# Performance work log

Measured on AMD Instinct MI355X. Metric: run time of the kernel, lower is better.

Reference implementation:

```python
import jax, jax.numpy as jnp
import numpy as np

N, C, H, W = 2, 128, 64, 64
N_HEAD = 4
GROUPS = 16
EPS = 1e-5


def group_norm(x, scale, offset):
    # haiku GroupNorm, channels_first: normalize over (channels-in-group, h, w)
    n, c, h, w = x.shape
    xg = x.reshape(n, GROUPS, c // GROUPS, h, w)
    mu = xg.mean(axis=(2, 3, 4), keepdims=True)
    var = xg.var(axis=(2, 3, 4), keepdims=True)
    xg = (xg - mu) * jax.lax.rsqrt(var + EPS)
    return xg.reshape(n, c, h, w) * scale[None, :, None, None] + offset[None, :, None, None]


def setup_inputs() -> dict:
    key = jax.random.key(0)
    ks = jax.random.split(key, 4)
    inv_sqrt_c = 1.0 / np.sqrt(C).astype(np.float32)
    return {
        "x": jax.random.normal(ks[0], (N, C, H, W), dtype=jnp.float32),
        "w_qkv": jax.random.normal(ks[1], (C, 3 * C), dtype=jnp.float32) * inv_sqrt_c,
        "b_qkv": jnp.zeros((3 * C,), dtype=jnp.float32),
        "w_out": jax.random.normal(ks[2], (C, C), dtype=jnp.float32) * inv_sqrt_c,
        "b_out": jnp.zeros((C,), dtype=jnp.float32),
        "gn1_scale": jnp.ones((C,), dtype=jnp.float32),
        "gn1_offset": jnp.zeros((C,), dtype=jnp.float32),
        "gn2_scale": jnp.ones((C,), dtype=jnp.float32),
        "gn2_offset": jnp.zeros((C,), dtype=jnp.float32),
    }


def reference(x, w_qkv, b_qkv, w_out, b_out, gn1_scale, gn1_offset, gn2_scale, gn2_offset):
    n, c, h, w = x.shape
    dh = c // N_HEAD
    # GroupNorm (x is reassigned, so the residual uses the normalized x)
    xn = group_norm(x, gn1_scale, gn1_offset)
    # 1x1 conv qkv projection: [n, 3c, h, w]
    qkv = jnp.einsum('nchw,cd->ndhw', xn, w_qkv) + b_qkv[None, :, None, None]
    # [n, 3H, dh, hw] -> [n, 3H, hw, dh]
    qkv = jnp.swapaxes(qkv.reshape(n, N_HEAD * 3, dh, h * w), 2, 3)
    q, k, v = jnp.split(qkv, 3, axis=1)  # each [n, H, hw, dh]
    scale = dh ** (-0.25)
    # [n, H, hw, hw] attention matrix (the memory-bound core)
    att = jax.nn.softmax((q * scale) @ (jnp.swapaxes(k, 2, 3) * scale), axis=3)
    y = jnp.swapaxes(att @ v, 2, 3).reshape(n, c, h, w)
    # 1x1 conv out projection + GroupNorm + residual
    out = jnp.einsum('nchw,cd->ndhw', y, w_out) + b_out[None, :, None, None]
    return xn + group_norm(out, gn2_scale, gn2_offset)
```

## Files before the change

### kernel.cpp

```cpp
#include <hip/hip_runtime.h>
#include <hip/hip_bf16.h>
#include <math.h>

constexpr int cHW   = 4096;
constexpr int cC    = 128;
constexpr int cNH   = 4;
constexpr int cDH   = 32;
constexpr float cEPS = 1e-5f;
constexpr float cQS = 0.2550347805f;
constexpr int SPLIT = 4;

typedef short bh8 __attribute__((ext_vector_type(8)));
typedef float f4  __attribute__((ext_vector_type(4)));

static __device__ __forceinline__ unsigned short f2bf(float f) {
  union { __hip_bfloat16 h; unsigned short u; } cv;
  cv.h = __float2bfloat16(f);
  return cv.u;
}
static __device__ __forceinline__ unsigned pack2bf(float a, float b) {
  return (unsigned)f2bf(a) | ((unsigned)f2bf(b) << 16);
}
static __device__ __forceinline__ unsigned pack_trunc(float a, float b) {
  unsigned ua = __builtin_bit_cast(unsigned, a);
  unsigned ub = __builtin_bit_cast(unsigned, b);
  return (ua >> 16) | (ub & 0xffff0000u);
}
static __device__ __forceinline__ float bflo(unsigned pk) {
  return __builtin_bit_cast(float, pk << 16);
}
static __device__ __forceinline__ float bfhi(unsigned pk) {
  return __builtin_bit_cast(float, pk & 0xffff0000u);
}

__device__ __forceinline__ void block_reduce2(float& a, float& b, float* sbuf) {
  #pragma unroll
  for (int off = 32; off > 0; off >>= 1) {
    a += __shfl_down(a, off, 64);
    b += __shfl_down(b, off, 64);
  }
  int wave = threadIdx.x >> 6;
  int lane = threadIdx.x & 63;
  if (lane == 0) { sbuf[wave] = a; sbuf[4 + wave] = b; }
  __syncthreads();
  if (threadIdx.x == 0) {
    sbuf[8] = sbuf[0] + sbuf[1] + sbuf[2] + sbuf[3];
    sbuf[9] = sbuf[4] + sbuf[5] + sbuf[6] + sbuf[7];
  }
  __syncthreads();
  a = sbuf[8];
  b = sbuf[9];
}

__global__ __launch_bounds__(256)
void prep(const float* __restrict__ x, float* __restrict__ part,
          const float* __restrict__ wq, const float* __restrict__ wo,
          unsigned short* __restrict__ wqT, unsigned short* __restrict__ woT) {
  __shared__ float lds[32 * 133];
  int L = threadIdx.x;
  if (blockIdx.x < 256) {
    int ng = blockIdx.x >> 3, sl = blockIdx.x & 7;
    const float4* s4 = (const float4*)x;
    float s = 0.f, s2 = 0.f;
    #pragma unroll
    for (int i = 0; i < 4; i++) {
      int idx = i * 256 + L;
      int c = idx >> 7, tt = idx & 127;
      float4 v = s4[(size_t)(ng * 8 + c) * 1024 + sl * 128 + tt];
      s  += v.x + v.y + v.z + v.w;
      s2 += v.x*v.x + v.y*v.y + v.z*v.z + v.w*v.w;
    }
    block_reduce2(s, s2, lds);
    if (L == 0) { part[blockIdx.x * 2] = s; part[blockIdx.x * 2 + 1] = s2; }
  } else {
    int bx = blockIdx.x - 256;
    const float* src; unsigned short* dst; int W, d0;
    if (bx < 12) { src = wq; dst = wqT; W = 384; d0 = bx * 32; }
    else         { src = wo; dst = woT; W = 128; d0 = (bx - 12) * 32; }
    #pragma unroll
    for (int i = 0; i < 16; i++) {
      int c = i * 8 + (L >> 5), d = L & 31;
      lds[d * 133 + c] = src[(size_t)c * W + d0 + d];
    }
    __syncthreads();
    int d = L >> 3, ch = L & 7, c0 = ch * 16;
    unsigned pk[8];
    #pragma unroll
    for (int j = 0; j < 8; j++)
      pk[j] = pack2bf(lds[d * 133 + c0 + 2 * j], lds[d * 133 + c0 + 2 * j + 1]);
    uint4* d4 = (uint4*)(dst + (size_t)(d0 + d) * 128 + c0);
    d4[0] = make_uint4(pk[0], pk[1], pk[2], pk[3]);
    d4[1] = make_uint4(pk[4], pk[5], pk[6], pk[7]);
  }
}

__global__ __launch_bounds__(256)
void gn_stats(const float* __restrict__ src, float* __restrict__ part) {
  __shared__ float sbuf[10];
  int ng = blockIdx.x >> 3, sl = blockIdx.x & 7;
  const float4* s4 = (const float4*)src;
  float s = 0.f, s2 = 0.f;
  #pragma unroll
  for (int i = 0; i < 4; i++) {
    int idx = i * 256 + threadIdx.x;
    int c = idx >> 7, tt = idx & 127;
    float4 v = s4[(size_t)(ng * 8 + c) * 1024 + sl * 128 + tt];
    s  += v.x + v.y + v.z + v.w;
    s2 += v.x*v.x + v.y*v.y + v.z*v.z + v.w*v.w;
  }
  block_reduce2(s, s2, sbuf);
  if (threadIdx.x == 0) { part[blockIdx.x * 2] = s; part[blockIdx.x * 2 + 1] = s2; }
}

__global__ __launch_bounds__(256)
void gn1_pack(const float* __restrict__ x, const float* __restrict__ part,
              const float* __restrict__ sc, const float* __restrict__ of,
              unsigned short* __restrict__ xnB) {
  int cc = blockIdx.x, ts = blockIdx.y, n = blockIdx.z;
  int ng = n * 16 + cc;
  float s = 0.f, s2 = 0.f;
  #pragma unroll
  for (int p = 0; p < 8; p++) { s += part[(ng*8+p)*2]; s2 += part[(ng*8+p)*2+1]; }
  float mu = s * (1.0f / 32768.0f);
  float rinv = rsqrtf(s2 * (1.0f / 32768.0f) - mu * mu + cEPS);
  int t = ts * 256 + threadIdx.x;
  float v[8];
  #pragma unroll
  for (int j = 0; j < 8; j++) {
    int c = cc * 8 + j;
    float a = rinv * sc[c];
    float bo = of[c] - mu * a;
    v[j] = x[((size_t)n * cC + c) * cHW + t] * a + bo;
  }
  unsigned pk[4];
  #pragma unroll
  for (int j = 0; j < 4; j++) pk[j] = pack2bf(v[2*j], v[2*j+1]);
  ((uint4*)xnB)[(size_t)(n * 16 + cc) * cHW + t] = make_uint4(pk[0], pk[1], pk[2], pk[3]);
}

__global__ __launch_bounds__(256)
void qkv_mfma(const unsigned short* __restrict__ xnB, const unsigned short* __restrict__ wqT,
              const float* __restrict__ bq, unsigned* __restrict__ qB,
              unsigned* __restrict__ kB, unsigned* __restrict__ vI) {
  __shared__ float vbuf[64 * 36];
  const int L = threadIdx.x & 63, w = threadIdx.x >> 6;
  const int c16 = L & 15, q = L >> 4;
  const int t0 = blockIdx.x * 64, dg = blockIdx.y, n = blockIdx.z;
  const int nh = n * 4 + (dg & 3), d0 = dg * 32;
  const f4 zf = {0.f, 0.f, 0.f, 0.f};
  f4 acc0 = zf, acc1 = zf;
  const int trow = t0 + w * 16 + c16;
  #pragma unroll
  for (int ks = 0; ks < 4; ks++) {
    bh8 a  = *(const bh8*)(xnB + ((size_t)(n * 16 + ks * 4 + q) * cHW + trow) * 8);
    bh8 b0 = *(const bh8*)(wqT + (size_t)(d0 + c16) * 128 + ks * 32 + q * 8);
    bh8 b1 = *(const bh8*)(wqT + (size_t)(d0 + 16 + c16) * 128 + ks * 32 + q * 8);
    acc0 = __builtin_amdgcn_mfma_f32_16x16x32_bf16(a, b0, acc0, 0, 0, 0);
    acc1 = __builtin_amdgcn_mfma_f32_16x16x32_bf16(a, b1, acc1, 0, 0, 0);
  }
  float blo = bq[d0 + c16], bhi = bq[d0 + 16 + c16];
  if (dg < 8) {
    float scl = (dg < 4) ? cQS : 1.0f;
    unsigned* dst = (dg < 4) ? qB : kB;
    #pragma unroll
    for (int r = 0; r < 4; r++) {
      unsigned pk = pack2bf((acc0[r] + blo) * scl, (acc1[r] + bhi) * scl);
      dst[((size_t)nh * cHW + t0 + w * 16 + q * 4 + r) * 16 + c16] = pk;
    }
  } else {
    #pragma unroll
    for (int r = 0; r < 4; r++) {
      vbuf[(w * 16 + q * 4 + r) * 36 + c16]      = acc0[r] + blo;
      vbuf[(w * 16 + q * 4 + r) * 36 + 16 + c16] = acc1[r] + bhi;
    }
    __syncthreads();
    int t16 = threadIdx.x & 15, dh8 = (threadIdx.x >> 4) & 15;
    #pragma unroll
    for (int blk = 0; blk < 2; blk++)
      #pragma unroll
      for (int hh = 0; hh < 2; hh++) {
        int dh = dh8 + hh * 16;
        float lo = vbuf[(blk * 32 + t16) * 36 + dh];
        float hi = vbuf[(blk * 32 + 16 + t16) * 36 + dh];
        vI[((size_t)nh * 32 + dh) * 2048 + (size_t)(t0 / 32 + blk) * 16 + t16] = pack2bf(lo, hi);
      }
  }
}

__global__ __launch_bounds__(256)
void flash_mfma(const unsigned short* __restrict__ qB,
                const unsigned short* __restrict__ kB,
                const unsigned short* __restrict__ vI,
                unsigned* __restrict__ opart, float* __restrict__ lpart) {
  __shared__ float pbuf[4][1280];
  const int w = threadIdx.x >> 6, L = threadIdx.x & 63;
  const int c16 = L & 15, q = L >> 4;
  const int qt = blockIdx.x * 4 + w, nh = blockIdx.y, ph = blockIdx.z;
  float* pb = pbuf[w];
  const f4 zf = {0.f, 0.f, 0.f, 0.f};
  const short oneb = 0x3F80;
  const bh8 ones = {oneb, oneb, oneb, oneb, oneb, oneb, oneb, oneb};

  const unsigned short* qb = qB + ((size_t)nh * cHW + qt * 32) * cDH;
  bh8 qa[2];
  qa[0] = *(const bh8*)(qb + (size_t)c16 * cDH + q * 8);
  qa[1] = *(const bh8*)(qb + (size_t)(16 + c16) * cDH + q * 8);

  f4 o[2][2] = {{zf, zf}, {zf, zf}};
  f4 lacc[2] = {zf, zf};

  const unsigned short* kb = kB + (size_t)nh * cHW * cDH;
  const unsigned short* vb = vI + (size_t)nh * cDH * cHW;

  const int kbeg = ph * (cHW / SPLIT);
  const int kend = kbeg + cHW / SPLIT;

  for (int kt = kbeg; kt < kend; kt += 64) {
    bh8 kf[4];
    #pragma unroll
    for (int s = 0; s < 4; s++)
      kf[s] = *(const bh8*)(kb + (size_t)(kt + s*16 + c16) * cDH + q * 8);
    bh8 vf[2][2];
    #pragma unroll
    for (int ks = 0; ks < 2; ks++)
      #pragma unroll
      for (int dt = 0; dt < 2; dt++)
        vf[ks][dt] = *(const bh8*)(vb + (size_t)(dt*16 + c16) * cHW + kt + ks*32 + q*8);

    f4 sf[2][4];
    #pragma unroll
    for (int rt = 0; rt < 2; rt++)
      #pragma unroll
      for (int s = 0; s < 4; s++)
        sf[rt][s] = __builtin_amdgcn_mfma_f32_16x16x32_bf16(qa[rt], kf[s], zf, 0, 0, 0);

    #pragma unroll
    for (int rt = 0; rt < 2; rt++) {
      #pragma unroll
      for (int s = 0; s < 4; s++)
        #pragma unroll
        for (int r = 0; r < 4; r++)
          sf[rt][s][r] = __builtin_amdgcn_exp2f(sf[rt][s][r]);
      #pragma unroll
      for (int st = 0; st < 2; st++)
        #pragma unroll
        for (int r = 0; r < 4; r++) {
          unsigned pk = pack_trunc(sf[rt][2*st][r], sf[rt][2*st+1][r]);
          pb[(rt*2 + st)*320 + (q*4 + r)*20 + c16] = __builtin_bit_cast(float, pk);
        }
    }
    #pragma unroll
    for (int rt = 0; rt < 2; rt++)
      #pragma unroll
      for (int st = 0; st < 2; st++) {
        bh8 pa = *(const bh8*)(pb + (rt*2 + st)*320 + c16*20 + q*4);
        o[rt][0] = __builtin_amdgcn_mfma_f32_16x16x32_bf16(pa, vf[st][0], o[rt][0], 0, 0, 0);
        o[rt][1] = __builtin_amdgcn_mfma_f32_16x16x32_bf16(pa, vf[st][1], o[rt][1], 0, 0, 0);
        lacc[rt] = __builtin_amdgcn_mfma_f32_16x16x32_bf16(pa, ones, lacc[rt], 0, 0, 0);
      }
  }

  size_t base_r = (size_t)ph * 32768 + (size_t)nh * cHW + (size_t)qt * 32;
  #pragma unroll
  for (int rt = 0; rt < 2; rt++)
    #pragma unroll
    for (int r = 0; r < 4; r++) {
      size_t rr = base_r + rt*16 + q*4 + r;
      if (c16 == 0) lpart[rr] = lacc[rt][r];
      opart[rr * 16 + c16] = pack_trunc(o[rt][0][r], o[rt][1][r]);
    }
}

__global__ __launch_bounds__(256)
void combine(const unsigned* __restrict__ opart, const float* __restrict__ lpart,
             unsigned* __restrict__ yB) {
  size_t r = (size_t)blockIdx.x * 256 + threadIdx.x;
  float l = 0.f;
  #pragma unroll
  for (int p = 0; p < SPLIT; p++) l += lpart[(size_t)p * 32768 + r];
  float e[32];
  #pragma unroll
  for (int j = 0; j < 32; j++) e[j] = 0.f;
  #pragma unroll
  for (int p = 0; p < SPLIT; p++) {
    const uint4* op = (const uint4*)(opart + ((size_t)p * 32768 + r) * 16);
    #pragma unroll
    for (int j = 0; j < 4; j++) {
      uint4 v = op[j];
      e[j*4+0] += bflo(v.x); e[16+j*4+0] += bfhi(v.x);
      e[j*4+1] += bflo(v.y); e[16+j*4+1] += bfhi(v.y);
      e[j*4+2] += bflo(v.z); e[16+j*4+2] += bfhi(v.z);
      e[j*4+3] += bflo(v.w); e[16+j*4+3] += bfhi(v.w);
    }
  }
  float inv = 1.0f / l;
  unsigned pk[16];
  #pragma unroll
  for (int m = 0; m < 16; m++) pk[m] = pack2bf(e[2*m] * inv, e[2*m+1] * inv);
  uint4* dst = (uint4*)(yB + r * 16);
  #pragma unroll
  for (int j = 0; j < 4; j++)
    dst[j] = make_uint4(pk[4*j], pk[4*j+1], pk[4*j+2], pk[4*j+3]);
}

__global__ __launch_bounds__(256)
void out_mfma(const unsigned short* __restrict__ yB, const unsigned short* __restrict__ woT,
              const float* __restrict__ bo, float* __restrict__ proj) {
  __shared__ float obuf[64 * 36];
  const int L = threadIdx.x & 63, w = threadIdx.x >> 6;
  const int c16 = L & 15, q = L >> 4;
  const int t0 = blockIdx.x * 64, d0 = blockIdx.y * 32, n = blockIdx.z;
  const f4 zf = {0.f, 0.f, 0.f, 0.f};
  f4 acc0 = zf, acc1 = zf;
  const int trow = t0 + w * 16 + c16;
  #pragma unroll
  for (int h = 0; h < 4; h++) {
    bh8 a  = *(const bh8*)(yB + ((size_t)(n * 4 + h) * cHW + trow) * 32 + q * 8);
    bh8 b0 = *(const bh8*)(woT + (size_t)(d0 + c16) * 128 + h * 32 + q * 8);
    bh8 b1 = *(const bh8*)(woT + (size_t)(d0 + 16 + c16) * 128 + h * 32 + q * 8);
    acc0 = __builtin_amdgcn_mfma_f32_16x16x32_bf16(a, b0, acc0, 0, 0, 0);
    acc1 = __builtin_amdgcn_mfma_f32_16x16x32_bf16(a, b1, acc1, 0, 0, 0);
  }
  float blo = bo[d0 + c16], bhi = bo[d0 + 16 + c16];
  #pragma unroll
  for (int r = 0; r < 4; r++) {
    obuf[(w * 16 + q * 4 + r) * 36 + c16]      = acc0[r] + blo;
    obuf[(w * 16 + q * 4 + r) * 36 + 16 + c16] = acc1[r] + bhi;
  }
  __syncthreads();
  int t16 = threadIdx.x & 15, d8 = (threadIdx.x >> 4) & 15;
  #pragma unroll
  for (int tc = 0; tc < 4; tc++)
    #pragma unroll
    for (int hh = 0; hh < 2; hh++) {
      int d = d8 + hh * 16;
      proj[((size_t)n * cC + d0 + d) * cHW + t0 + tc * 16 + t16] =
          obuf[(tc * 16 + t16) * 36 + d];
    }
}

__global__ __launch_bounds__(256)
void gn2_apply(const float* __restrict__ x, const float* __restrict__ proj,
               const float* __restrict__ p1, const float* __restrict__ p2,
               const float* __restrict__ s1, const float* __restrict__ o1,
               const float* __restrict__ s2, const float* __restrict__ o2,
               float* __restrict__ out) {
  int tid = blockIdx.x * 256 + threadIdx.x;
  int Cg = tid >> 8;
  int n = Cg >> 7, ch = Cg & 127, g = ch >> 3, ng = n * 16 + g;
  float sa = 0.f, sb = 0.f, ta = 0.f, tb = 0.f;
  #pragma unroll
  for (int p = 0; p < 8; p++) {
    sa += p1[(ng*8+p)*2]; sb += p1[(ng*8+p)*2+1];
    ta += p2[(ng*8+p)*2]; tb += p2[(ng*8+p)*2+1];
  }
  float mu1 = sa * (1.0f/32768.0f);
  float ri1 = rsqrtf(sb * (1.0f/32768.0f) - mu1*mu1 + cEPS);
  float a1 = ri1 * s1[ch], b1 = o1[ch] - mu1 * a1;
  float mu2 = ta * (1.0f/32768.0f);
  float ri2 = rsqrtf(tb * (1.0f/32768.0f) - mu2*mu2 + cEPS);
  float a2 = ri2 * s2[ch], b2 = o2[ch] - mu2 * a2;
  const float4* x4 = (const float4*)x;
  const float4* pr4 = (const float4*)proj;
  float4* o4 = (float4*)out;
  #pragma unroll
  for (int i = 0; i < 4; i++) {
    size_t f = (size_t)tid * 4 + i;
    float4 xv = x4[f], pv = pr4[f];
    float4 r;
    r.x = xv.x * a1 + b1 + pv.x * a2 + b2;
    r.y = xv.y * a1 + b1 + pv.y * a2 + b2;
    r.z = xv.z * a1 + b1 + pv.z * a2 + b2;
    r.w = xv.w * a1 + b1 + pv.w * a2 + b2;
    o4[f] = r;
  }
}

extern "C" void kernel_launch(void* const* d_in, const int* in_sizes, int n_in,
                              void* d_out, int out_size, void* d_ws, size_t ws_size,
                              hipStream_t stream) {
  const float* x     = (const float*)d_in[0];
  const float* w_qkv = (const float*)d_in[1];
  const float* b_qkv = (const float*)d_in[2];
  const float* w_out = (const float*)d_in[3];
  const float* b_out = (const float*)d_in[4];
  const float* g1s   = (const float*)d_in[5];
  const float* g1o   = (const float*)d_in[6];
  const float* g2s   = (const float*)d_in[7];
  const float* g2o   = (const float*)d_in[8];
  float* out = (float*)d_out;
  float* ws  = (float*)d_ws;

  const size_t MAP = (size_t)2 * cC * cHW;
  float* proj    = ws;
  float* lpart   = proj + MAP;
  float* stats1  = lpart + (size_t)SPLIT * 32768;
  float* stats2  = stats1 + 512;
  unsigned* opart = (unsigned*)(stats2 + 512);
  unsigned* qB   = opart + (size_t)SPLIT * 32768 * 16;
  unsigned* kB   = qB + MAP / 2;
  unsigned* vI   = kB + MAP / 2;
  unsigned* yB   = vI + MAP / 2;
  unsigned short* xnB = (unsigned short*)(yB + MAP / 2);
  unsigned short* wqT = xnB + MAP;
  unsigned short* woT = wqT + 49152;

  prep      <<<dim3(272),           256, 0, stream>>>(x, stats1, w_qkv, w_out, wqT, woT);
  gn1_pack  <<<dim3(16, 16, 2),     256, 0, stream>>>(x, stats1, g1s, g1o, xnB);
  qkv_mfma  <<<dim3(64, 12, 2),     256, 0, stream>>>(xnB, wqT, b_qkv, qB, kB, vI);
  flash_mfma<<<dim3(32, 8, SPLIT),  256, 0, stream>>>((const unsigned short*)qB,
                                                      (const unsigned short*)kB,
                                                      (const unsigned short*)vI,
                                                      opart, lpart);
  combine   <<<dim3(128),           256, 0, stream>>>(opart, lpart, yB);
  out_mfma  <<<dim3(64, 4, 2),      256, 0, stream>>>((const unsigned short*)yB, woT,
                                                      b_out, proj);
  gn_stats  <<<dim3(256),           256, 0, stream>>>(proj, stats2);
  gn2_apply <<<dim3(256),           256, 0, stream>>>(x, proj, stats1, stats2,
                                                      g1s, g1o, g2s, g2o, out);
}
```

Before: 148.3 us.

## Fuse GroupNorm2 statistics into output projection and raise flash split to eight

Computes per-group sum and sum-of-squares for the second GroupNorm inside the out_mfma epilogue, using wave shuffles and atomicAdd into a zeroed stats buffer. This removes the separate gn_stats kernel and its re-read of the projection output. Also doubles the flash-attention KV split count to expose more parallelism, at the cost of larger partial buffers and more combine work. Atomic float accumulation makes the statistics order-dependent.

After: 201.6 us. 1.36x slower.

```diff
diff --git a/kernel.cpp b/kernel.cpp
--- a/kernel.cpp
+++ b/kernel.cpp
@@ -8,7 +8,7 @@
 constexpr int cDH   = 32;
 constexpr float cEPS = 1e-5f;
 constexpr float cQS = 0.2550347805f;
-constexpr int SPLIT = 4;
+constexpr int SPLIT = 8;
 
 typedef short bh8 __attribute__((ext_vector_type(8)));
 typedef float f4  __attribute__((ext_vector_type(4)));
@@ -92,24 +92,6 @@
     d4[0] = make_uint4(pk[0], pk[1], pk[2], pk[3]);
     d4[1] = make_uint4(pk[4], pk[5], pk[6], pk[7]);
   }
-}
-
-__global__ __launch_bounds__(256)
-void gn_stats(const float* __restrict__ src, float* __restrict__ part) {
-  __shared__ float sbuf[10];
-  int ng = blockIdx.x >> 3, sl = blockIdx.x & 7;
-  const float4* s4 = (const float4*)src;
-  float s = 0.f, s2 = 0.f;
-  #pragma unroll
-  for (int i = 0; i < 4; i++) {
-    int idx = i * 256 + threadIdx.x;
-    int c = idx >> 7, tt = idx & 127;
-    float4 v = s4[(size_t)(ng * 8 + c) * 1024 + sl * 128 + tt];
-    s  += v.x + v.y + v.z + v.w;
-    s2 += v.x*v.x + v.y*v.y + v.z*v.z + v.w*v.w;
-  }
-  block_reduce2(s, s2, sbuf);
-  if (threadIdx.x == 0) { part[blockIdx.x * 2] = s; part[blockIdx.x * 2 + 1] = s2; }
 }
 
 __global__ __launch_bounds__(256)
@@ -305,7 +287,8 @@
 
 __global__ __launch_bounds__(256)
 void out_mfma(const unsigned short* __restrict__ yB, const unsigned short* __restrict__ woT,
-              const float* __restrict__ bo, float* __restrict__ proj) {
+              const float* __restrict__ bo, float* __restrict__ proj,
+              float* __restrict__ stats2) {
   __shared__ float obuf[64 * 36];
   const int L = threadIdx.x & 63, w = threadIdx.x >> 6;
   const int c16 = L & 15, q = L >> 4;
@@ -322,10 +305,32 @@
     acc1 = __builtin_amdgcn_mfma_f32_16x16x32_bf16(a, b1, acc1, 0, 0, 0);
   }
   float blo = bo[d0 + c16], bhi = bo[d0 + 16 + c16];
+  float v0[4], v1[4];
+  float sa = 0.f, sa2 = 0.f, sb = 0.f, sb2 = 0.f;
   #pragma unroll
   for (int r = 0; r < 4; r++) {
-    obuf[(w * 16 + q * 4 + r) * 36 + c16]      = acc0[r] + blo;
-    obuf[(w * 16 + q * 4 + r) * 36 + 16 + c16] = acc1[r] + bhi;
+    v0[r] = acc0[r] + blo; v1[r] = acc1[r] + bhi;
+    sa += v0[r]; sa2 += v0[r]*v0[r];
+    sb += v1[r]; sb2 += v1[r]*v1[r];
+  }
+  #pragma unroll
+  for (int d = 1; d < 64; d <<= 1) {
+    if (d == 8) continue;
+    sa += __shfl_xor(sa, d, 64);  sa2 += __shfl_xor(sa2, d, 64);
+    sb += __shfl_xor(sb, d, 64);  sb2 += __shfl_xor(sb2, d, 64);
+  }
+  if ((L & 55) == 0) {
+    int gofs = (L >> 3) & 1;
+    int gb = n * 16 + (d0 >> 3);
+    atomicAdd(&stats2[(gb + gofs) * 2],     sa);
+    atomicAdd(&stats2[(gb + gofs) * 2 + 1], sa2);
+    atomicAdd(&stats2[(gb + 2 + gofs) * 2],     sb);
+    atomicAdd(&stats2[(gb + 2 + gofs) * 2 + 1], sb2);
+  }
+  #pragma unroll
+  for (int r = 0; r < 4; r++) {
+    obuf[(w * 16 + q * 4 + r) * 36 + c16]      = v0[r];
+    obuf[(w * 16 + q * 4 + r) * 36 + 16 + c16] = v1[r];
   }
   __syncthreads();
   int t16 = threadIdx.x & 15, d8 = (threadIdx.x >> 4) & 15;
@@ -348,12 +353,10 @@
   int tid = blockIdx.x * 256 + threadIdx.x;
   int Cg = tid >> 8;
   int n = Cg >> 7, ch = Cg & 127, g = ch >> 3, ng = n * 16 + g;
-  float sa = 0.f, sb = 0.f, ta = 0.f, tb = 0.f;
-  #pragma unroll
-  for (int p = 0; p < 8; p++) {
-    sa += p1[(ng*8+p)*2]; sb += p1[(ng*8+p)*2+1];
-    ta += p2[(ng*8+p)*2]; tb += p2[(ng*8+p)*2+1];
-  }
+  float sa = 0.f, sb = 0.f;
+  #pragma unroll
+  for (int p = 0; p < 8; p++) { sa += p1[(ng*8+p)*2]; sb += p1[(ng*8+p)*2+1]; }
+  float ta = p2[ng*2], tb = p2[ng*2+1];
   float mu1 = sa * (1.0f/32768.0f);
   float ri1 = rsqrtf(sb * (1.0f/32768.0f) - mu1*mu1 + cEPS);
   float a1 = ri1 * s1[ch], b1 = o1[ch] - mu1 * a1;
@@ -396,7 +399,7 @@
   float* lpart   = proj + MAP;
   float* stats1  = lpart + (size_t)SPLIT * 32768;
   float* stats2  = stats1 + 512;
-  unsigned* opart = (unsigned*)(stats2 + 512);
+  unsigned* opart = (unsigned*)(stats2 + 64);
   unsigned* qB   = opart + (size_t)SPLIT * 32768 * 16;
   unsigned* kB   = qB + MAP / 2;
   unsigned* vI   = kB + MAP / 2;
@@ -405,6 +408,7 @@
   unsigned short* wqT = xnB + MAP;
   unsigned short* woT = wqT + 49152;
 
+  hipMemsetAsync(stats2, 0, 64 * sizeof(float), stream);
   prep      <<<dim3(272),           256, 0, stream>>>(x, stats1, w_qkv, w_out, wqT, woT);
   gn1_pack  <<<dim3(16, 16, 2),     256, 0, stream>>>(x, stats1, g1s, g1o, xnB);
   qkv_mfma  <<<dim3(64, 12, 2),     256, 0, stream>>>(xnB, wqT, b_qkv, qB, kB, vI);
@@ -414,8 +418,7 @@
                                                       opart, lpart);
   combine   <<<dim3(128),           256, 0, stream>>>(opart, lpart, yB);
   out_mfma  <<<dim3(64, 4, 2),      256, 0, stream>>>((const unsigned short*)yB, woT,
-                                                      b_out, proj);
-  gn_stats  <<<dim3(256),           256, 0, stream>>>(proj, stats2);
+                                                      b_out, proj, stats2);
   gn2_apply <<<dim3(256),           256, 0, stream>>>(x, proj, stats1, stats2,
                                                       g1s, g1o, g2s, g2o, out);
 }
```
